# Optimization experiments

Measured on AMD Instinct MI355X. Metric: run time of the kernel, lower is better.

## Reference

```python
import jax, jax.numpy as jnp
import numpy as np

N = 50000   # nodes
E = 800000  # edges
G = 64      # graphs
D_IN = 128
H = 128
H2 = 64  # max(H//2, 8)
H3 = 32  # max(H//4, 8)
OUT = 2
EPS = 1e-5


def setup_inputs() -> dict:
    key = jax.random.key(0)
    ks = jax.random.split(key, 32)

    def w(k, shape, scale=0.05):
        return jax.random.normal(k, shape, dtype=jnp.float32) * scale

    inp = {
        "x": jax.random.normal(ks[0], (N, D_IN), dtype=jnp.float32),
        "edge_src": jax.random.randint(ks[1], (E,), 0, N, dtype=jnp.int32),
        "edge_dst": jax.random.randint(ks[2], (E,), 0, N, dtype=jnp.int32),
        "edge_weight": jax.random.uniform(ks[3], (E,), dtype=jnp.float32),
        "batch": jnp.sort(jax.random.randint(ks[4], (N,), 0, G, dtype=jnp.int32)),
        # GCNConv weights/biases
        "W1": w(ks[5], (D_IN, H)), "b1": jnp.zeros((H,), jnp.float32),
        "W2": w(ks[6], (H, H)),    "b2": jnp.zeros((H,), jnp.float32),
        "W3": w(ks[7], (H, H)),    "b3": jnp.zeros((H,), jnp.float32),
        # BatchNorm affine params
        "g1": jnp.ones((H,), jnp.float32), "be1": jnp.zeros((H,), jnp.float32),
        "g2": jnp.ones((H,), jnp.float32), "be2": jnp.zeros((H,), jnp.float32),
        "g3": jnp.ones((H,), jnp.float32), "be3": jnp.zeros((H,), jnp.float32),
        # MLP head
        "Wm1": w(ks[8], (H, H)),   "bm1": jnp.zeros((H,), jnp.float32),
        "Wm2": w(ks[9], (H, H2)),  "bm2": jnp.zeros((H2,), jnp.float32),
        "Wm3": w(ks[10], (H2, H3)), "bm3": jnp.zeros((H3,), jnp.float32),
        "Wm4": w(ks[11], (H3, OUT)), "bm4": jnp.zeros((OUT,), jnp.float32),
    }
    return inp


def reference(x, edge_src, edge_dst, edge_weight, batch,
              W1, b1, W2, b2, W3, b3,
              g1, be1, g2, be2, g3, be3,
              Wm1, bm1, Wm2, bm2, Wm3, bm3, Wm4, bm4):
    n = x.shape[0]
    loop = jnp.arange(n, dtype=edge_src.dtype)
    # PyG GCNConv default: add self-loops with weight 1, symmetric normalization
    src = jnp.concatenate([edge_src, loop])
    dst = jnp.concatenate([edge_dst, loop])
    w = jnp.concatenate([edge_weight, jnp.ones((n,), x.dtype)])
    deg = jax.ops.segment_sum(w, dst, num_segments=n)              # [N]
    dinv = jnp.where(deg > 0, deg ** -0.5, 0.0)
    norm = dinv[src] * w * dinv[dst]                               # [E+N]

    def gcn_conv(h, W, b):
        h = h @ W                                                  # [N, H]
        msg = norm[:, None] * h[src]                               # gather + scale
        return jax.ops.segment_sum(msg, dst, num_segments=n) + b   # scatter-add

    def bn(h, gamma, beta):
        mu = h.mean(axis=0)
        var = ((h - mu) ** 2).mean(axis=0)   # biased var, as torch BN training
        return (h - mu) * jax.lax.rsqrt(var + EPS) * gamma + beta

    h = jax.nn.relu(bn(gcn_conv(x, W1, b1), g1, be1))
    h = jax.nn.relu(bn(gcn_conv(h, W2, b2), g2, be2))
    h = jax.nn.relu(bn(gcn_conv(h, W3, b3), g3, be3))

    # global mean pool over graphs
    counts = jax.ops.segment_sum(jnp.ones((n,), h.dtype), batch, num_segments=G)
    pooled = jax.ops.segment_sum(h, batch, num_segments=G) / jnp.maximum(counts, 1.0)[:, None]

    # MLP head
    z = jax.nn.relu(pooled @ Wm1 + bm1)
    z = jax.nn.relu(z @ Wm2 + bm2)
    z = jax.nn.relu(z @ Wm3 + bm3)
    return z @ Wm4 + bm4
```

## Files before the change

### kernel.cpp

```cpp
#include <hip/hip_runtime.h>
#include <hip/hip_bf16.h>

#define NN 50000
#define NE 800000
#define NG 64
#define DH 128
#define EPSV 1e-5
#define NBLK_AGG 1000
#define NPB 50
#define SCAN_BLK 256
#define SCAN_NBLK ((NN + SCAN_BLK - 1) / SCAN_BLK)
#define PB_STRIDE 1024


__global__ void edge_count(const int* __restrict__ dst, int* __restrict__ ecnt,
                           int* __restrict__ off) {
    int e = blockIdx.x * 256 + threadIdx.x;
    if (e < NE) off[e] = atomicAdd(&ecnt[dst[e]], 1);
}

__global__ __launch_bounds__(SCAN_BLK) void scan_partial(
    const int* __restrict__ ecnt, int* __restrict__ bsum) {
    int tid = threadIdx.x;
    int i = blockIdx.x * SCAN_BLK + tid;
    int v = (i < NN) ? ecnt[i] : 0;
    __shared__ int sm[SCAN_BLK];
    sm[tid] = v;
    __syncthreads();
    for (int off = SCAN_BLK / 2; off > 0; off >>= 1) {
        if (tid < off) sm[tid] += sm[tid + off];
        __syncthreads();
    }
    if (tid == 0) bsum[blockIdx.x] = sm[0];
}

__global__ __launch_bounds__(256) void scan_bsum_gc(
    const int* __restrict__ bsum, int* __restrict__ boff,
    const int* __restrict__ batch, int* __restrict__ cnt) {
    int tid = threadIdx.x;
    int v = (tid < SCAN_NBLK) ? bsum[tid] : 0;
    __shared__ int s[256];
    s[tid] = v;
    __syncthreads();
    for (int off = 1; off < 256; off <<= 1) {
        int u = (tid >= off) ? s[tid - off] : 0;
        __syncthreads();
        s[tid] += u;
        __syncthreads();
    }
    if (tid < SCAN_NBLK) boff[tid] = s[tid] - v;
    if (tid < NG) {
        auto lb = [&](int key) {
            int lo = 0, hi = NN;
            while (lo < hi) { int mid = (lo + hi) >> 1; if (batch[mid] < key) lo = mid + 1; else hi = mid; }
            return lo;
        };
        cnt[tid] = lb(tid + 1) - lb(tid);
    }
}

__global__ __launch_bounds__(SCAN_BLK) void rowptr_write(
    const int* __restrict__ ecnt, const int* __restrict__ boff,
    int* __restrict__ rowptr) {
    int tid = threadIdx.x;
    int i = blockIdx.x * SCAN_BLK + tid;
    int v = (i < NN) ? ecnt[i] : 0;
    __shared__ int s[SCAN_BLK];
    s[tid] = v;
    __syncthreads();
    for (int off = 1; off < SCAN_BLK; off <<= 1) {
        int u = (tid >= off) ? s[tid - off] : 0;
        __syncthreads();
        s[tid] += u;
        __syncthreads();
    }
    if (i < NN) rowptr[i] = s[tid] - v + boff[blockIdx.x];
    if (i == 0) rowptr[NN] = NE;
}

__global__ void edge_place2(const int* __restrict__ src, const int* __restrict__ dst,
                            const float* __restrict__ w, const int* __restrict__ rowptr,
                            const int* __restrict__ off, int* __restrict__ csr_src,
                            float* __restrict__ csr_w) {
    int e = blockIdx.x * 256 + threadIdx.x;
    if (e < NE) {
        int pos = rowptr[dst[e]] + off[e];
        csr_src[pos] = src[e];
        csr_w[pos] = w[e];
    }
}

__global__ void deg_dinv_csr(const float* __restrict__ csr_w,
                             const int* __restrict__ rowptr,
                             float* __restrict__ dinv) {
    int n = blockIdx.x * 256 + threadIdx.x;
    if (n < NN) {
        float s = 1.0f;
        int e1 = rowptr[n + 1];
        for (int e = rowptr[n]; e < e1; ++e) s += csr_w[e];
        dinv[n] = 1.0f / sqrtf(s);
    }
}

__global__ void norm_csr(const float* __restrict__ dinv, const int* __restrict__ rowptr,
                         const int* __restrict__ csr_src, float* __restrict__ csr_norm) {
    int n = blockIdx.x * 256 + threadIdx.x;
    if (n < NN) {
        float dn = dinv[n];
        int e1 = rowptr[n + 1];
        for (int e = rowptr[n]; e < e1; ++e)
            csr_norm[e] = dinv[csr_src[e]] * csr_norm[e] * dn;
    }
}


__global__ __launch_bounds__(256) void gemm_fused(
    const float* __restrict__ hin, const float* __restrict__ scale,
    const float* __restrict__ shift, const float* __restrict__ W,
    __hip_bfloat162* __restrict__ hwb)
{
    __shared__ float Ws[DH * DH];
    __shared__ float hs[32 * DH];
    int tid = threadIdx.x;

    const float4* Wg = (const float4*)W;
    float4* Ws4 = (float4*)Ws;
#pragma unroll
    for (int i = 0; i < 16; ++i) Ws4[tid + i * 256] = Wg[tid + i * 256];

    int row0 = blockIdx.x * 32;
    float4* hs4 = (float4*)hs;
#pragma unroll
    for (int i = 0; i < 4; ++i) {
        int f4 = tid + i * 256;
        int r = f4 >> 5;
        int c4 = f4 & 31;
        int row = row0 + r;
        float4 v = make_float4(0.f, 0.f, 0.f, 0.f);
        if (row < NN) {
            v = ((const float4*)hin)[row * 32 + c4];
            if (scale) {
                int c = c4 * 4;
                v.x = fmaxf(v.x * scale[c + 0] + shift[c + 0], 0.f);
                v.y = fmaxf(v.y * scale[c + 1] + shift[c + 1], 0.f);
                v.z = fmaxf(v.z * scale[c + 2] + shift[c + 2], 0.f);
                v.w = fmaxf(v.w * scale[c + 3] + shift[c + 3], 0.f);
            }
        }
        hs4[f4] = v;
    }
    __syncthreads();

    int ct = tid & 31;
    int rg = tid >> 5;
    float4 acc0 = make_float4(0, 0, 0, 0), acc1 = acc0, acc2 = acc0, acc3 = acc0;

#pragma unroll 8
    for (int k = 0; k < DH; ++k) {
        float4 wv = Ws4[k * 32 + ct];
        float a0 = hs[(rg * 4 + 0) * DH + k];
        float a1 = hs[(rg * 4 + 1) * DH + k];
        float a2 = hs[(rg * 4 + 2) * DH + k];
        float a3 = hs[(rg * 4 + 3) * DH + k];
        acc0.x += a0 * wv.x; acc0.y += a0 * wv.y; acc0.z += a0 * wv.z; acc0.w += a0 * wv.w;
        acc1.x += a1 * wv.x; acc1.y += a1 * wv.y; acc1.z += a1 * wv.z; acc1.w += a1 * wv.w;
        acc2.x += a2 * wv.x; acc2.y += a2 * wv.y; acc2.z += a2 * wv.z; acc2.w += a2 * wv.w;
        acc3.x += a3 * wv.x; acc3.y += a3 * wv.y; acc3.z += a3 * wv.z; acc3.w += a3 * wv.w;
    }

    float4 accs[4] = {acc0, acc1, acc2, acc3};
#pragma unroll
    for (int j = 0; j < 4; ++j) {
        int row = row0 + rg * 4 + j;
        if (row < NN) {
            hwb[row * 64 + ct * 2 + 0] =
                __float22bfloat162_rn(make_float2(accs[j].x, accs[j].y));
            hwb[row * 64 + ct * 2 + 1] =
                __float22bfloat162_rn(make_float2(accs[j].z, accs[j].w));
        }
    }
}


__global__ __launch_bounds__(512) void agg_csr(
    const __hip_bfloat162* __restrict__ hwb, const int* __restrict__ rowptr,
    const int* __restrict__ csr_src, const float* __restrict__ csr_norm,
    const float* __restrict__ b, const float* __restrict__ dinv,
    float2* __restrict__ agg2, double* __restrict__ pblock_t)
{
    int tid = threadIdx.x;
    int lane = tid & 63;
    int w = tid >> 6;
    float2 bb = ((const float2*)b)[lane];
    double sx = 0.0, sy = 0.0, qx = 0.0, qy = 0.0;
    int n0 = blockIdx.x * NPB;
    int n1 = min(n0 + NPB, NN);
    for (int node = n0 + w; node < n1; node += 8) {
        float di = dinv[node];
        float d2 = di * di;
        float2 h = __bfloat1622float2(hwb[node * 64 + lane]);
        float accx = h.x * d2 + bb.x;
        float accy = h.y * d2 + bb.y;
        int e = rowptr[node], e1 = rowptr[node + 1];
        for (; e + 8 <= e1; e += 8) {
            int a0 = csr_src[e + 0];
            int a1 = csr_src[e + 1];
            int a2 = csr_src[e + 2];
            int a3 = csr_src[e + 3];
            int a4 = csr_src[e + 4];
            int a5 = csr_src[e + 5];
            int a6 = csr_src[e + 6];
            int a7 = csr_src[e + 7];
            float w0 = csr_norm[e + 0];
            float w1 = csr_norm[e + 1];
            float w2 = csr_norm[e + 2];
            float w3 = csr_norm[e + 3];
            float w4 = csr_norm[e + 4];
            float w5 = csr_norm[e + 5];
            float w6 = csr_norm[e + 6];
            float w7 = csr_norm[e + 7];
            float2 v0 = __bfloat1622float2(hwb[a0 * 64 + lane]);
            float2 v1 = __bfloat1622float2(hwb[a1 * 64 + lane]);
            float2 v2 = __bfloat1622float2(hwb[a2 * 64 + lane]);
            float2 v3 = __bfloat1622float2(hwb[a3 * 64 + lane]);
            float2 v4 = __bfloat1622float2(hwb[a4 * 64 + lane]);
            float2 v5 = __bfloat1622float2(hwb[a5 * 64 + lane]);
            float2 v6 = __bfloat1622float2(hwb[a6 * 64 + lane]);
            float2 v7 = __bfloat1622float2(hwb[a7 * 64 + lane]);
            accx += w0 * v0.x; accy += w0 * v0.y;
            accx += w1 * v1.x; accy += w1 * v1.y;
            accx += w2 * v2.x; accy += w2 * v2.y;
            accx += w3 * v3.x; accy += w3 * v3.y;
            accx += w4 * v4.x; accy += w4 * v4.y;
            accx += w5 * v5.x; accy += w5 * v5.y;
            accx += w6 * v6.x; accy += w6 * v6.y;
            accx += w7 * v7.x; accy += w7 * v7.y;
        }
        for (; e + 4 <= e1; e += 4) {
            int a0 = csr_src[e + 0];
            int a1 = csr_src[e + 1];
            int a2 = csr_src[e + 2];
            int a3 = csr_src[e + 3];
            float w0 = csr_norm[e + 0];
            float w1 = csr_norm[e + 1];
            float w2 = csr_norm[e + 2];
            float w3 = csr_norm[e + 3];
            float2 v0 = __bfloat1622float2(hwb[a0 * 64 + lane]);
            float2 v1 = __bfloat1622float2(hwb[a1 * 64 + lane]);
            float2 v2 = __bfloat1622float2(hwb[a2 * 64 + lane]);
            float2 v3 = __bfloat1622float2(hwb[a3 * 64 + lane]);
            accx += w0 * v0.x; accy += w0 * v0.y;
            accx += w1 * v1.x; accy += w1 * v1.y;
            accx += w2 * v2.x; accy += w2 * v2.y;
            accx += w3 * v3.x; accy += w3 * v3.y;
        }
        for (; e < e1; ++e) {
            float wn = csr_norm[e];
            float2 v = __bfloat1622float2(hwb[csr_src[e] * 64 + lane]);
            accx += wn * v.x; accy += wn * v.y;
        }
        agg2[node * 64 + lane] = make_float2(accx, accy);
        sx += (double)accx; qx += (double)accx * (double)accx;
        sy += (double)accy; qy += (double)accy * (double)accy;
    }
    __shared__ double shx[8][64], shy[8][64], qhx[8][64], qhy[8][64];
    shx[w][lane] = sx; shy[w][lane] = sy;
    qhx[w][lane] = qx; qhy[w][lane] = qy;
    __syncthreads();
    if (tid < 128) {
        int d = tid;
        int ls = d >> 1;
        int comp = d & 1;
        double ssum = 0.0, qsum = 0.0;
#pragma unroll
        for (int ww = 0; ww < 8; ++ww) {
            ssum += comp ? shy[ww][ls] : shx[ww][ls];
            qsum += comp ? qhy[ww][ls] : qhx[ww][ls];
        }
        pblock_t[d * PB_STRIDE + blockIdx.x]         = ssum;
        pblock_t[(128 + d) * PB_STRIDE + blockIdx.x] = qsum;
    }
}

__global__ __launch_bounds__(256) void bn_reduce_t(
    const double* __restrict__ pblock_t, const float* __restrict__ g,
    const float* __restrict__ be, float* __restrict__ scale,
    float* __restrict__ shift)
{
    int d = blockIdx.x;
    int tid = threadIdx.x;
    double s = 0.0, q = 0.0;
    for (int i = tid; i < NBLK_AGG; i += 256) {
        s += pblock_t[d * PB_STRIDE + i];
        q += pblock_t[(128 + d) * PB_STRIDE + i];
    }
    __shared__ double ss[256], qq[256];
    ss[tid] = s; qq[tid] = q;
    __syncthreads();
    for (int off = 128; off > 0; off >>= 1) {
        if (tid < off) { ss[tid] += ss[tid + off]; qq[tid] += qq[tid + off]; }
        __syncthreads();
    }
    if (tid == 0) {
        double mu = ss[0] / (double)NN;
        double ex2 = qq[0] / (double)NN;
        double var = ex2 - mu * mu;
        double sc = (double)g[d] / sqrt(var + (double)EPSV);
        scale[d] = (float)sc;
        shift[d] = (float)((double)be[d] - mu * sc);
    }
}


#define POOL_CHUNK 100
__global__ __launch_bounds__(256) void pool_k(
    const float* __restrict__ agg, const float* __restrict__ scale,
    const float* __restrict__ shift, const int* __restrict__ batch,
    double* __restrict__ pooled)
{
    int tid = threadIdx.x;
    int d = tid & 127;
    int rl = tid >> 7;
    float sc = scale[d], sh = shift[d];
    int r0 = blockIdx.x * POOL_CHUNK;
    int rend = r0 + POOL_CHUNK;
    if (rend > NN) rend = NN;
    double acc = 0.0;
    int gc = -1;
    for (int r = r0 + rl; r < rend; r += 2) {
        int g = batch[r];
        float v = agg[r * DH + d];
        v = fmaxf(v * sc + sh, 0.f);
        if (g != gc) {
            if (gc >= 0) unsafeAtomicAdd(&pooled[gc * DH + d], acc);
            gc = g; acc = 0.0;
        }
        acc += (double)v;
    }
    if (gc >= 0) unsafeAtomicAdd(&pooled[gc * DH + d], acc);
}


__global__ __launch_bounds__(128) void mlp_k(
    const double* __restrict__ pooled, const int* __restrict__ cnt,
    const float* __restrict__ Wm1, const float* __restrict__ bm1,
    const float* __restrict__ Wm2, const float* __restrict__ bm2,
    const float* __restrict__ Wm3, const float* __restrict__ bm3,
    const float* __restrict__ Wm4, const float* __restrict__ bm4,
    float* __restrict__ out)
{
    int g = blockIdx.x;
    int tid = threadIdx.x;
    __shared__ float za[DH], zb[DH];
    float cf = fmaxf((float)cnt[g], 1.0f);
    za[tid] = (float)(pooled[g * DH + tid] / (double)cf);
    __syncthreads();
    float acc = bm1[tid];
    for (int k = 0; k < 128; ++k) acc += za[k] * Wm1[k * 128 + tid];
    zb[tid] = fmaxf(acc, 0.f);
    __syncthreads();
    if (tid < 64) {
        acc = bm2[tid];
        for (int k = 0; k < 128; ++k) acc += zb[k] * Wm2[k * 64 + tid];
        za[tid] = fmaxf(acc, 0.f);
    }
    __syncthreads();
    if (tid < 32) {
        acc = bm3[tid];
        for (int k = 0; k < 64; ++k) acc += za[k] * Wm3[k * 32 + tid];
        zb[tid] = fmaxf(acc, 0.f);
    }
    __syncthreads();
    if (tid < 2) {
        acc = bm4[tid];
        for (int k = 0; k < 32; ++k) acc += zb[k] * Wm4[k * 2 + tid];
        out[g * 2 + tid] = acc;
    }
}


extern "C" void kernel_launch(void* const* d_in, const int* in_sizes, int n_in,
                              void* d_out, int out_size, void* d_ws, size_t ws_size,
                              hipStream_t stream) {
    const float* x  = (const float*)d_in[0];
    const int* esrc = (const int*)d_in[1];
    const int* edst = (const int*)d_in[2];
    const float* ew = (const float*)d_in[3];
    const int* batch = (const int*)d_in[4];
    const float* W1 = (const float*)d_in[5];  const float* b1 = (const float*)d_in[6];
    const float* W2 = (const float*)d_in[7];  const float* b2 = (const float*)d_in[8];
    const float* W3 = (const float*)d_in[9];  const float* b3 = (const float*)d_in[10];
    const float* g1 = (const float*)d_in[11]; const float* be1 = (const float*)d_in[12];
    const float* g2 = (const float*)d_in[13]; const float* be2 = (const float*)d_in[14];
    const float* g3 = (const float*)d_in[15]; const float* be3 = (const float*)d_in[16];
    const float* Wm1 = (const float*)d_in[17]; const float* bm1 = (const float*)d_in[18];
    const float* Wm2 = (const float*)d_in[19]; const float* bm2 = (const float*)d_in[20];
    const float* Wm3 = (const float*)d_in[21]; const float* bm3 = (const float*)d_in[22];
    const float* Wm4 = (const float*)d_in[23]; const float* bm4 = (const float*)d_in[24];
    float* out = (float*)d_out;

    char* ws = (char*)d_ws;
    int*    ecnt   = (int*)(ws + 0);
    double* pooled = (double*)(ws + 200192);
    float*  dinv   = (float*)(ws + 265728);
    int*    cnt    = (int*)(ws + 465728);
    float*  scale0 = (float*)(ws + 465984);
    int*    bsum   = (int*)(ws + 469056);
    int*    boff   = (int*)(ws + 470080);
    int*    rowptr = (int*)(ws + 471104);
    int*    csr_src  = (int*)(ws + 671744);
    float*  csr_norm = (float*)(ws + 3871744);
    double* pblock_t = (double*)(ws + 7071744);
    __hip_bfloat162* hwb = (__hip_bfloat162*)(ws + 9323648);
    float*  aggA   = (float*)(ws + 34923648);
    float*  aggB   = (float*)(ws + 60523648);
    int*    off    = (int*)(ws + 60523648);

    hipMemsetAsync(d_ws, 0, 265728, stream);

    edge_count<<<(NE + 255) / 256, 256, 0, stream>>>(edst, ecnt, off);
    scan_partial<<<SCAN_NBLK, SCAN_BLK, 0, stream>>>(ecnt, bsum);
    scan_bsum_gc<<<1, 256, 0, stream>>>(bsum, boff, batch, cnt);
    rowptr_write<<<SCAN_NBLK, SCAN_BLK, 0, stream>>>(ecnt, boff, rowptr);
    edge_place2<<<(NE + 255) / 256, 256, 0, stream>>>(esrc, edst, ew, rowptr, off,
                                                      csr_src, csr_norm);
    deg_dinv_csr<<<(NN + 255) / 256, 256, 0, stream>>>(csr_norm, rowptr, dinv);
    norm_csr<<<(NN + 255) / 256, 256, 0, stream>>>(dinv, rowptr, csr_src, csr_norm);

    const float* Ws_[3] = {W1, W2, W3};
    const float* bs_[3] = {b1, b2, b3};
    const float* gs_[3] = {g1, g2, g3};
    const float* bes_[3] = {be1, be2, be3};
    float* aggs[3] = {aggA, aggB, aggA};
    const int gemm_grid = (NN + 31) / 32;

    const float* curIn = x;
    const float* curScale = nullptr;
    const float* curShift = nullptr;
    for (int l = 0; l < 3; ++l) {
        float* agg = aggs[l];
        gemm_fused<<<gemm_grid, 256, 0, stream>>>(curIn, curScale, curShift,
                                                  Ws_[l], hwb);
        agg_csr<<<NBLK_AGG, 512, 0, stream>>>(hwb, rowptr, csr_src,
                                              csr_norm, bs_[l], dinv,
                                              (float2*)agg, pblock_t);
        float* sc = scale0 + l * 256;
        float* sh = sc + 128;
        bn_reduce_t<<<128, 256, 0, stream>>>(pblock_t, gs_[l], bes_[l], sc, sh);
        curIn = agg;
        curScale = sc;
        curShift = sh;
    }

    pool_k<<<(NN + POOL_CHUNK - 1) / POOL_CHUNK, 256, 0, stream>>>(
        aggA, curScale, curShift, batch, pooled);
    mlp_k<<<NG, 128, 0, stream>>>(pooled, cnt, Wm1, bm1, Wm2, bm2, Wm3, bm3,
                                  Wm4, bm4, out);
}
```

Measured before the change: 444.1 us.

## Factor GCN normalization into GEMM/aggregation and fuse scan and pool+MLP kernels

Drops the per-edge normalization kernel by pre-scaling GEMM outputs by dinv[src] and scaling aggregated sums by dinv[dst], using raw edge weights in aggregation. Merges the block-offset scan into the rowptr kernel and fuses graph pooling with the MLP head, with one block per graph finding its node range by binary search. This cuts launches, per-edge memory traffic and atomics. Pooling now runs on only 64 blocks, which may limit parallelism.

```diff
diff --git a/kernel.cpp b/kernel.cpp
--- a/kernel.cpp
+++ b/kernel.cpp
@@ -34,38 +34,24 @@
     if (tid == 0) bsum[blockIdx.x] = sm[0];
 }
 
-__global__ __launch_bounds__(256) void scan_bsum_gc(
-    const int* __restrict__ bsum, int* __restrict__ boff,
-    const int* __restrict__ batch, int* __restrict__ cnt) {
-    int tid = threadIdx.x;
-    int v = (tid < SCAN_NBLK) ? bsum[tid] : 0;
-    __shared__ int s[256];
-    s[tid] = v;
+__global__ __launch_bounds__(SCAN_BLK) void rowptr_write_f(
+    const int* __restrict__ ecnt, const int* __restrict__ bsum,
+    int* __restrict__ rowptr) {
+    __shared__ int sb[256];
+    __shared__ int s[SCAN_BLK];
+    int tid = threadIdx.x;
+    int bv = (tid < SCAN_NBLK) ? bsum[tid] : 0;
+    sb[tid] = bv;
     __syncthreads();
     for (int off = 1; off < 256; off <<= 1) {
-        int u = (tid >= off) ? s[tid - off] : 0;
-        __syncthreads();
-        s[tid] += u;
-        __syncthreads();
-    }
-    if (tid < SCAN_NBLK) boff[tid] = s[tid] - v;
-    if (tid < NG) {
-        auto lb = [&](int key) {
-            int lo = 0, hi = NN;
-            while (lo < hi) { int mid = (lo + hi) >> 1; if (batch[mid] < key) lo = mid + 1; else hi = mid; }
-            return lo;
-        };
-        cnt[tid] = lb(tid + 1) - lb(tid);
-    }
-}
-
-__global__ __launch_bounds__(SCAN_BLK) void rowptr_write(
-    const int* __restrict__ ecnt, const int* __restrict__ boff,
-    int* __restrict__ rowptr) {
-    int tid = threadIdx.x;
+        int u = (tid >= off) ? sb[tid - off] : 0;
+        __syncthreads();
+        sb[tid] += u;
+        __syncthreads();
+    }
+    int boff = (blockIdx.x > 0) ? sb[blockIdx.x - 1] : 0;
     int i = blockIdx.x * SCAN_BLK + tid;
     int v = (i < NN) ? ecnt[i] : 0;
-    __shared__ int s[SCAN_BLK];
     s[tid] = v;
     __syncthreads();
     for (int off = 1; off < SCAN_BLK; off <<= 1) {
@@ -74,7 +60,7 @@
         s[tid] += u;
         __syncthreads();
     }
-    if (i < NN) rowptr[i] = s[tid] - v + boff[blockIdx.x];
+    if (i < NN) rowptr[i] = s[tid] - v + boff;
     if (i == 0) rowptr[NN] = NE;
 }
 
@@ -102,22 +88,11 @@
     }
 }
 
-__global__ void norm_csr(const float* __restrict__ dinv, const int* __restrict__ rowptr,
-                         const int* __restrict__ csr_src, float* __restrict__ csr_norm) {
-    int n = blockIdx.x * 256 + threadIdx.x;
-    if (n < NN) {
-        float dn = dinv[n];
-        int e1 = rowptr[n + 1];
-        for (int e = rowptr[n]; e < e1; ++e)
-            csr_norm[e] = dinv[csr_src[e]] * csr_norm[e] * dn;
-    }
-}
-
 
 __global__ __launch_bounds__(256) void gemm_fused(
     const float* __restrict__ hin, const float* __restrict__ scale,
     const float* __restrict__ shift, const float* __restrict__ W,
-    __hip_bfloat162* __restrict__ hwb)
+    const float* __restrict__ dinv, __hip_bfloat162* __restrict__ hwb)
 {
     __shared__ float Ws[DH * DH];
     __shared__ float hs[32 * DH];
@@ -173,10 +148,11 @@
     for (int j = 0; j < 4; ++j) {
         int row = row0 + rg * 4 + j;
         if (row < NN) {
+            float di = dinv[row];
             hwb[row * 64 + ct * 2 + 0] =
-                __float22bfloat162_rn(make_float2(accs[j].x, accs[j].y));
+                __float22bfloat162_rn(make_float2(accs[j].x * di, accs[j].y * di));
             hwb[row * 64 + ct * 2 + 1] =
-                __float22bfloat162_rn(make_float2(accs[j].z, accs[j].w));
+                __float22bfloat162_rn(make_float2(accs[j].z * di, accs[j].w * di));
         }
     }
 }
@@ -184,7 +160,7 @@
 
 __global__ __launch_bounds__(512) void agg_csr(
     const __hip_bfloat162* __restrict__ hwb, const int* __restrict__ rowptr,
-    const int* __restrict__ csr_src, const float* __restrict__ csr_norm,
+    const int* __restrict__ csr_src, const float* __restrict__ csr_w,
     const float* __restrict__ b, const float* __restrict__ dinv,
     float2* __restrict__ agg2, double* __restrict__ pblock_t)
 {
@@ -197,10 +173,9 @@
     int n1 = min(n0 + NPB, NN);
     for (int node = n0 + w; node < n1; node += 8) {
         float di = dinv[node];
-        float d2 = di * di;
         float2 h = __bfloat1622float2(hwb[node * 64 + lane]);
-        float accx = h.x * d2 + bb.x;
-        float accy = h.y * d2 + bb.y;
+        float accx = h.x;
+        float accy = h.y;
         int e = rowptr[node], e1 = rowptr[node + 1];
         for (; e + 8 <= e1; e += 8) {
             int a0 = csr_src[e + 0];
@@ -211,14 +186,14 @@
             int a5 = csr_src[e + 5];
             int a6 = csr_src[e + 6];
             int a7 = csr_src[e + 7];
-            float w0 = csr_norm[e + 0];
-            float w1 = csr_norm[e + 1];
-            float w2 = csr_norm[e + 2];
-            float w3 = csr_norm[e + 3];
-            float w4 = csr_norm[e + 4];
-            float w5 = csr_norm[e + 5];
-            float w6 = csr_norm[e + 6];
-            float w7 = csr_norm[e + 7];
+            float w0 = csr_w[e + 0];
+            float w1 = csr_w[e + 1];
+            float w2 = csr_w[e + 2];
+            float w3 = csr_w[e + 3];
+            float w4 = csr_w[e + 4];
+            float w5 = csr_w[e + 5];
+            float w6 = csr_w[e + 6];
+            float w7 = csr_w[e + 7];
             float2 v0 = __bfloat1622float2(hwb[a0 * 64 + lane]);
             float2 v1 = __bfloat1622float2(hwb[a1 * 64 + lane]);
             float2 v2 = __bfloat1622float2(hwb[a2 * 64 + lane]);
@@ -241,10 +216,10 @@
             int a1 = csr_src[e + 1];
             int a2 = csr_src[e + 2];
             int a3 = csr_src[e + 3];
-            float w0 = csr_norm[e + 0];
-            float w1 = csr_norm[e + 1];
-            float w2 = csr_norm[e + 2];
-            float w3 = csr_norm[e + 3];
+            float w0 = csr_w[e + 0];
+            float w1 = csr_w[e + 1];
+            float w2 = csr_w[e + 2];
+            float w3 = csr_w[e + 3];
             float2 v0 = __bfloat1622float2(hwb[a0 * 64 + lane]);
             float2 v1 = __bfloat1622float2(hwb[a1 * 64 + lane]);
             float2 v2 = __bfloat1622float2(hwb[a2 * 64 + lane]);
@@ -255,13 +230,15 @@
             accx += w3 * v3.x; accy += w3 * v3.y;
         }
         for (; e < e1; ++e) {
-            float wn = csr_norm[e];
+            float wn = csr_w[e];
             float2 v = __bfloat1622float2(hwb[csr_src[e] * 64 + lane]);
             accx += wn * v.x; accy += wn * v.y;
         }
-        agg2[node * 64 + lane] = make_float2(accx, accy);
-        sx += (double)accx; qx += (double)accx * (double)accx;
-        sy += (double)accy; qy += (double)accy * (double)accy;
+        float ox = accx * di + bb.x;
+        float oy = accy * di + bb.y;
+        agg2[node * 64 + lane] = make_float2(ox, oy);
+        sx += (double)ox; qx += (double)ox * (double)ox;
+        sy += (double)oy; qy += (double)oy * (double)oy;
     }
     __shared__ double shx[8][64], shy[8][64], qhx[8][64], qhy[8][64];
     shx[w][lane] = sx; shy[w][lane] = sy;
@@ -312,37 +289,9 @@
 }
 
 
-#define POOL_CHUNK 100
-__global__ __launch_bounds__(256) void pool_k(
+__global__ __launch_bounds__(256) void pool_mlp(
     const float* __restrict__ agg, const float* __restrict__ scale,
     const float* __restrict__ shift, const int* __restrict__ batch,
-    double* __restrict__ pooled)
-{
-    int tid = threadIdx.x;
-    int d = tid & 127;
-    int rl = tid >> 7;
-    float sc = scale[d], sh = shift[d];
-    int r0 = blockIdx.x * POOL_CHUNK;
-    int rend = r0 + POOL_CHUNK;
-    if (rend > NN) rend = NN;
-    double acc = 0.0;
-    int gc = -1;
-    for (int r = r0 + rl; r < rend; r += 2) {
-        int g = batch[r];
-        float v = agg[r * DH + d];
-        v = fmaxf(v * sc + sh, 0.f);
-        if (g != gc) {
-            if (gc >= 0) unsafeAtomicAdd(&pooled[gc * DH + d], acc);
-            gc = g; acc = 0.0;
-        }
-        acc += (double)v;
-    }
-    if (gc >= 0) unsafeAtomicAdd(&pooled[gc * DH + d], acc);
-}
-
-
-__global__ __launch_bounds__(128) void mlp_k(
-    const double* __restrict__ pooled, const int* __restrict__ cnt,
     const float* __restrict__ Wm1, const float* __restrict__ bm1,
     const float* __restrict__ Wm2, const float* __restrict__ bm2,
     const float* __restrict__ Wm3, const float* __restrict__ bm3,
@@ -351,30 +300,52 @@
 {
     int g = blockIdx.x;
     int tid = threadIdx.x;
+    auto lb = [&](int key) {
+        int lo = 0, hi = NN;
+        while (lo < hi) { int mid = (lo + hi) >> 1; if (batch[mid] < key) lo = mid + 1; else hi = mid; }
+        return lo;
+    };
+    int lo = lb(g), hi = lb(g + 1);
+
+    int d = tid & 127;
+    int half = tid >> 7;
+    float sc = scale[d], sh = shift[d];
+    double acc = 0.0;
+    for (int r = lo + half; r < hi; r += 2)
+        acc += (double)fmaxf(agg[r * DH + d] * sc + sh, 0.f);
+
+    __shared__ double pm[256];
     __shared__ float za[DH], zb[DH];
-    float cf = fmaxf((float)cnt[g], 1.0f);
-    za[tid] = (float)(pooled[g * DH + tid] / (double)cf);
-    __syncthreads();
-    float acc = bm1[tid];
-    for (int k = 0; k < 128; ++k) acc += za[k] * Wm1[k * 128 + tid];
-    zb[tid] = fmaxf(acc, 0.f);
+    pm[tid] = acc;
+    __syncthreads();
+    if (tid < 128) {
+        double cf = (double)((hi - lo) > 0 ? (hi - lo) : 1);
+        za[tid] = (float)((pm[tid] + pm[tid + 128]) / cf);
+    }
+    __syncthreads();
+    float a;
+    if (tid < 128) {
+        a = bm1[tid];
+        for (int k = 0; k < 128; ++k) a += za[k] * Wm1[k * 128 + tid];
+        zb[tid] = fmaxf(a, 0.f);
+    }
     __syncthreads();
     if (tid < 64) {
-        acc = bm2[tid];
-        for (int k = 0; k < 128; ++k) acc += zb[k] * Wm2[k * 64 + tid];
-        za[tid] = fmaxf(acc, 0.f);
+        a = bm2[tid];
+        for (int k = 0; k < 128; ++k) a += zb[k] * Wm2[k * 64 + tid];
+        za[tid] = fmaxf(a, 0.f);
     }
     __syncthreads();
     if (tid < 32) {
-        acc = bm3[tid];
-        for (int k = 0; k < 64; ++k) acc += za[k] * Wm3[k * 32 + tid];
-        zb[tid] = fmaxf(acc, 0.f);
+        a = bm3[tid];
+        for (int k = 0; k < 64; ++k) a += za[k] * Wm3[k * 32 + tid];
+        zb[tid] = fmaxf(a, 0.f);
     }
     __syncthreads();
     if (tid < 2) {
-        acc = bm4[tid];
-        for (int k = 0; k < 32; ++k) acc += zb[k] * Wm4[k * 2 + tid];
-        out[g * 2 + tid] = acc;
+        a = bm4[tid];
+        for (int k = 0; k < 32; ++k) a += zb[k] * Wm4[k * 2 + tid];
+        out[g * 2 + tid] = a;
     }
 }
 
@@ -401,31 +372,26 @@
 
     char* ws = (char*)d_ws;
     int*    ecnt   = (int*)(ws + 0);
-    double* pooled = (double*)(ws + 200192);
-    float*  dinv   = (float*)(ws + 265728);
-    int*    cnt    = (int*)(ws + 465728);
-    float*  scale0 = (float*)(ws + 465984);
-    int*    bsum   = (int*)(ws + 469056);
-    int*    boff   = (int*)(ws + 470080);
-    int*    rowptr = (int*)(ws + 471104);
-    int*    csr_src  = (int*)(ws + 671744);
-    float*  csr_norm = (float*)(ws + 3871744);
-    double* pblock_t = (double*)(ws + 7071744);
-    __hip_bfloat162* hwb = (__hip_bfloat162*)(ws + 9323648);
-    float*  aggA   = (float*)(ws + 34923648);
-    float*  aggB   = (float*)(ws + 60523648);
-    int*    off    = (int*)(ws + 60523648);
-
-    hipMemsetAsync(d_ws, 0, 265728, stream);
+    float*  dinv   = (float*)(ws + 200192);
+    float*  scale0 = (float*)(ws + 400384);
+    int*    bsum   = (int*)(ws + 403456);
+    int*    rowptr = (int*)(ws + 404480);
+    int*    csr_src = (int*)(ws + 604672);
+    float*  csr_w   = (float*)(ws + 3804672);
+    double* pblock_t = (double*)(ws + 7004672);
+    __hip_bfloat162* hwb = (__hip_bfloat162*)(ws + 9101824);
+    float*  aggA   = (float*)(ws + 21901824);
+    float*  aggB   = (float*)(ws + 47501824);
+    int*    off    = (int*)(ws + 47501824);
+
+    hipMemsetAsync(d_ws, 0, 200192, stream);
 
     edge_count<<<(NE + 255) / 256, 256, 0, stream>>>(edst, ecnt, off);
     scan_partial<<<SCAN_NBLK, SCAN_BLK, 0, stream>>>(ecnt, bsum);
-    scan_bsum_gc<<<1, 256, 0, stream>>>(bsum, boff, batch, cnt);
-    rowptr_write<<<SCAN_NBLK, SCAN_BLK, 0, stream>>>(ecnt, boff, rowptr);
+    rowptr_write_f<<<SCAN_NBLK, SCAN_BLK, 0, stream>>>(ecnt, bsum, rowptr);
     edge_place2<<<(NE + 255) / 256, 256, 0, stream>>>(esrc, edst, ew, rowptr, off,
-                                                      csr_src, csr_norm);
-    deg_dinv_csr<<<(NN + 255) / 256, 256, 0, stream>>>(csr_norm, rowptr, dinv);
-    norm_csr<<<(NN + 255) / 256, 256, 0, stream>>>(dinv, rowptr, csr_src, csr_norm);
+                                                      csr_src, csr_w);
+    deg_dinv_csr<<<(NN + 255) / 256, 256, 0, stream>>>(csr_w, rowptr, dinv);
 
     const float* Ws_[3] = {W1, W2, W3};
     const float* bs_[3] = {b1, b2, b3};
@@ -440,9 +406,9 @@
     for (int l = 0; l < 3; ++l) {
         float* agg = aggs[l];
         gemm_fused<<<gemm_grid, 256, 0, stream>>>(curIn, curScale, curShift,
-                                                  Ws_[l], hwb);
+                                                  Ws_[l], dinv, hwb);
         agg_csr<<<NBLK_AGG, 512, 0, stream>>>(hwb, rowptr, csr_src,
-                                              csr_norm, bs_[l], dinv,
+                                              csr_w, bs_[l], dinv,
                                               (float2*)agg, pblock_t);
         float* sc = scale0 + l * 256;
         float* sh = sc + 128;
@@ -452,8 +418,6 @@
         curShift = sh;
     }
 
-    pool_k<<<(NN + POOL_CHUNK - 1) / POOL_CHUNK, 256, 0, stream>>>(
-        aggA, curScale, curShift, batch, pooled);
-    mlp_k<<<NG, 128, 0, stream>>>(pooled, cnt, Wm1, bm1, Wm2, bm2, Wm3, bm3,
-                                  Wm4, bm4, out);
-}
+    pool_mlp<<<NG, 256, 0, stream>>>(aggA, curScale, curShift, batch,
+                                     Wm1, bm1, Wm2, bm2, Wm3, bm3, Wm4, bm4, out);
+}
```

After: 525.6 us. 18.3% more time.
